# Kernel tuning notes

Measured on AMD Instinct MI355X. Metric: run time of the kernel, lower is better.

Reference implementation:

```python
import jax, jax.numpy as jnp
import numpy as np

B, S, D, N, H = 4, 1024, 768, 12, 64
IGNORE = -100000.0


def setup_inputs() -> dict:
    key = jax.random.key(0)
    ks = jax.random.split(key, 9)
    std = 0.02
    return {
        "normalized_resid_pre": jax.random.normal(ks[0], (B, S, D), dtype=jnp.float32),
        "W_Q": jax.random.normal(ks[1], (N, D, H), dtype=jnp.float32) * std,
        "W_K": jax.random.normal(ks[2], (N, D, H), dtype=jnp.float32) * std,
        "W_V": jax.random.normal(ks[3], (N, D, H), dtype=jnp.float32) * std,
        "W_O": jax.random.normal(ks[4], (N, H, D), dtype=jnp.float32) * std,
        "b_Q": jnp.zeros((N, H), dtype=jnp.float32),
        "b_K": jnp.zeros((N, H), dtype=jnp.float32),
        "b_V": jnp.zeros((N, H), dtype=jnp.float32),
        "b_O": jnp.zeros((D,), dtype=jnp.float32),
    }


def reference(normalized_resid_pre, W_Q, W_K, W_V, W_O, b_Q, b_K, b_V, b_O):
    x = normalized_resid_pre  # [b, s, d]
    d_head = W_Q.shape[-1]
    # per-head projections: [b, n, s, h]
    Q = jnp.einsum("bsd,ndh->bnsh", x, W_Q) + b_Q[None, :, None, :]
    K = jnp.einsum("bsd,ndh->bnsh", x, W_K) + b_K[None, :, None, :]
    V = jnp.einsum("bsd,ndh->bnsh", x, W_V) + b_V[None, :, None, :]
    # scores [b, n, s_q, s_k]
    scores = jnp.einsum("bnqh,bnkh->bnqk", Q, K) / jnp.sqrt(jnp.float32(d_head))
    s = scores.shape[-1]
    # original: tril(scores) + triu(IGNORE, k=1) == where(causal, scores, IGNORE)
    causal = jnp.tril(jnp.ones((s, s), dtype=bool))
    masked = jnp.where(causal[None, None], scores, jnp.float32(IGNORE))
    probs = jax.nn.softmax(masked, axis=-1)
    # z [b, s_q, n, h]
    z = jnp.einsum("bnqk,bnkh->bqnh", probs, V)
    out = jnp.einsum("bqnh,nhd->bqd", z, W_O) + b_O
    return out
```

## Files before the change

### kernel.cpp

```cpp
#include <hip/hip_runtime.h>

typedef __bf16 bf16x8 __attribute__((ext_vector_type(8)));
typedef __bf16 bf16x4 __attribute__((ext_vector_type(4)));
typedef float  f32x4  __attribute__((ext_vector_type(4)));

constexpr int B_ = 4, S_ = 1024, D_ = 768, N_ = 12, H_ = 64;
constexpr int BNSH = B_ * N_ * S_ * H_;
constexpr float SCALE2 = 0.18033688011f;

__device__ __forceinline__ f32x4 mfma16(bf16x8 a, bf16x8 b, f32x4 c) {
    return __builtin_amdgcn_mfma_f32_16x16x32_bf16(a, b, c, 0, 0, 0);
}

__device__ __forceinline__ void gload16(const __bf16* g, __bf16* l) {
    __builtin_amdgcn_global_load_lds(
        (const __attribute__((address_space(1))) unsigned int*)g,
        (__attribute__((address_space(3))) unsigned int*)l, 16, 0, 0);
}

__device__ __forceinline__ void stage128x64(const __bf16* g, int ld, __bf16* lds,
                                            int wid, int lane) {
    #pragma unroll
    for (int i = 0; i < 4; ++i) {
        int cb = (wid * 4 + i) * 64;
        int chunk = cb + lane;
        int r = chunk >> 3, p = chunk & 7;
        int q = p ^ (r & 7);
        gload16(g + (size_t)r * ld + q * 8, lds + cb * 8);
    }
}
__device__ __forceinline__ void stage64x64(const __bf16* g, int ld, __bf16* lds,
                                           int wid, int lane) {
    #pragma unroll
    for (int i = 0; i < 2; ++i) {
        int cb = (wid * 2 + i) * 64;
        int chunk = cb + lane;
        int r = chunk >> 3, p = chunk & 7;
        int q = p ^ (r & 7);
        gload16(g + (size_t)r * ld + q * 8, lds + cb * 8);
    }
}

__global__ __launch_bounds__(256) void prep_kernel(
    const float* __restrict__ x,
    const float* __restrict__ wq, const float* __restrict__ wk,
    const float* __restrict__ wv, const float* __restrict__ wo,
    __bf16* __restrict__ xb, __bf16* __restrict__ wt, __bf16* __restrict__ wot) {
    __shared__ __bf16 T[64][65];
    const int blk = blockIdx.x;
    const int tid = threadIdx.x;
    if (blk < 768) {
        int base = blk * 1024 + tid;
        #pragma unroll
        for (int i = 0; i < 4; ++i) {
            int idx = base + i * 256;
            float4 v = ((const float4*)x)[idx];
            bf16x4 o;
            o[0] = (__bf16)v.x; o[1] = (__bf16)v.y;
            o[2] = (__bf16)v.z; o[3] = (__bf16)v.w;
            ((bf16x4*)xb)[idx] = o;
        }
        return;
    }
    int rr = tid >> 4, c4 = (tid & 15) * 4;
    if (blk < 1200) {
        int t = blk - 768;
        int dt = t % 12, mh = t / 12;
        int mat = mh / 12, n = mh % 12;
        const float* in = (mat == 0 ? wq : mat == 1 ? wk : wv) + (size_t)n * 768 * 64;
        __bf16* outp = wt + (size_t)(mat * 768 + n * 64) * 768;
        int d0 = dt * 64;
        #pragma unroll
        for (int i = 0; i < 4; ++i) {
            int row = rr + 16 * i;
            float4 v = *(const float4*)&in[(size_t)(d0 + row) * 64 + c4];
            T[c4 + 0][row] = (__bf16)v.x;
            T[c4 + 1][row] = (__bf16)v.y;
            T[c4 + 2][row] = (__bf16)v.z;
            T[c4 + 3][row] = (__bf16)v.w;
        }
        __syncthreads();
        #pragma unroll
        for (int i = 0; i < 4; ++i) {
            int hrow = rr + 16 * i;
            bf16x4 o;
            o[0] = T[hrow][c4 + 0]; o[1] = T[hrow][c4 + 1];
            o[2] = T[hrow][c4 + 2]; o[3] = T[hrow][c4 + 3];
            *(bf16x4*)&outp[(size_t)hrow * 768 + d0 + c4] = o;
        }
    } else {
        int t = blk - 1200;
        int r0 = (t % 12) * 64, c0 = (t / 12) * 64;
        #pragma unroll
        for (int i = 0; i < 4; ++i) {
            int row = rr + 16 * i;
            float4 v = *(const float4*)&wo[(size_t)(r0 + row) * 768 + c0 + c4];
            T[c4 + 0][row] = (__bf16)v.x;
            T[c4 + 1][row] = (__bf16)v.y;
            T[c4 + 2][row] = (__bf16)v.z;
            T[c4 + 3][row] = (__bf16)v.w;
        }
        __syncthreads();
        #pragma unroll
        for (int i = 0; i < 4; ++i) {
            int crow = rr + 16 * i;
            bf16x4 o;
            o[0] = T[crow][c4 + 0]; o[1] = T[crow][c4 + 1];
            o[2] = T[crow][c4 + 2]; o[3] = T[crow][c4 + 3];
            *(bf16x4*)&wot[(size_t)(c0 + crow) * 768 + r0 + c4] = o;
        }
    }
}

__global__ __launch_bounds__(256) void qkv_gemm(
    const __bf16* __restrict__ xb, const __bf16* __restrict__ wtg,
    const float* __restrict__ bq, const float* __restrict__ bk,
    const float* __restrict__ bv,
    __bf16* __restrict__ Qb, __bf16* __restrict__ Kb, __bf16* __restrict__ Vtb) {
    __shared__ __bf16 As[2][128 * 64];
    __shared__ __bf16 Bs[2][64 * 64];
    const int m0 = blockIdx.x * 128;
    const int j0 = blockIdx.y * 64;
    const int tid = threadIdx.x, wid = tid >> 6, lane = tid & 63;
    const int quad = lane >> 4, lrow = lane & 15;
    const int l3 = lrow & 7;
    int koff[2];
    #pragma unroll
    for (int ks = 0; ks < 2; ++ks)
        koff[ks] = lrow * 64 + ((ks * 4 + quad) ^ l3) * 8;

    f32x4 zf = {0.f, 0.f, 0.f, 0.f};
    f32x4 acc[2][4];
    #pragma unroll
    for (int i = 0; i < 2; ++i)
        #pragma unroll
        for (int j = 0; j < 4; ++j) acc[i][j] = zf;

    stage128x64(xb + (size_t)m0 * 768, 768, As[0], wid, lane);
    stage64x64(wtg + (size_t)j0 * 768, 768, Bs[0], wid, lane);

    for (int kt = 0; kt < 12; ++kt) {
        const int buf = kt & 1;
        __syncthreads();
        if (kt < 11) {
            stage128x64(xb + (size_t)m0 * 768 + (kt + 1) * 64, 768, As[buf ^ 1], wid, lane);
            stage64x64(wtg + (size_t)j0 * 768 + (kt + 1) * 64, 768, Bs[buf ^ 1], wid, lane);
        }
        #pragma unroll
        for (int ks = 0; ks < 2; ++ks) {
            bf16x8 af[2], bfr[4];
            #pragma unroll
            for (int mi = 0; mi < 2; ++mi)
                af[mi] = *(const bf16x8*)(As[buf] + (wid * 32 + mi * 16) * 64 + koff[ks]);
            #pragma unroll
            for (int ni = 0; ni < 4; ++ni)
                bfr[ni] = *(const bf16x8*)(Bs[buf] + ni * 1024 + koff[ks]);
            #pragma unroll
            for (int mi = 0; mi < 2; ++mi)
                #pragma unroll
                for (int ni = 0; ni < 4; ++ni)
                    acc[mi][ni] = mfma16(af[mi], bfr[ni], acc[mi][ni]);
        }
    }

    const int mat = j0 / 768;
    const int n = (j0 % 768) >> 6;
    const int b = m0 >> 10;
    const int s_base = (m0 & 1023) + wid * 32;
    const float* bias = (mat == 0 ? bq : mat == 1 ? bk : bv) + n * 64;
    const float osc = (mat == 0) ? SCALE2 : 1.0f;
    float bias_v[4];
    #pragma unroll
    for (int ni = 0; ni < 4; ++ni) bias_v[ni] = bias[ni * 16 + lrow];

    if (mat == 2) {
        __bf16* vout = Vtb + (size_t)(b * N_ + n) * 64 * 1024;
        #pragma unroll
        for (int mi = 0; mi < 2; ++mi)
            #pragma unroll
            for (int ni = 0; ni < 4; ++ni) {
                int h = ni * 16 + lrow;
                int s0 = s_base + mi * 16 + quad * 4;
                bf16x4 pv;
                #pragma unroll
                for (int r = 0; r < 4; ++r)
                    pv[r] = (__bf16)(acc[mi][ni][r] + bias_v[ni]);
                *(bf16x4*)(vout + (size_t)h * 1024 + s0) = pv;
            }
    } else {
        __bf16* qk = (mat == 0 ? Qb : Kb) + (size_t)(b * N_ + n) * 1024 * 64;
        #pragma unroll
        for (int mi = 0; mi < 2; ++mi)
            #pragma unroll
            for (int r = 0; r < 4; ++r) {
                int s = s_base + mi * 16 + quad * 4 + r;
                #pragma unroll
                for (int ni = 0; ni < 4; ++ni)
                    qk[(size_t)s * 64 + ni * 16 + lrow] =
                        (__bf16)((acc[mi][ni][r] + bias_v[ni]) * osc);
            }
    }
}

__global__ __launch_bounds__(256) void attn_mfma(
    const __bf16* __restrict__ Qb, const __bf16* __restrict__ Kb,
    const __bf16* __restrict__ Vtb, __bf16* __restrict__ zb) {
    __shared__ __bf16 Ks[2][64 * 64], Vs[2][64 * 64];
    __shared__ __bf16 Pt[4][16 * 64];
    const int bid = blockIdx.x;
    const int qt = 15 - bid / 48;
    const int bn = bid % 48;
    const int b = bn / N_, n = bn % N_;
    const int tid = threadIdx.x, wid = tid >> 6, lane = tid & 63;
    const int quad = lane >> 4, lrow = lane & 15;
    const int l3 = lrow & 7;
    const __bf16* Qg = Qb + (size_t)(b * N_ + n) * S_ * H_;
    const __bf16* Kg = Kb + (size_t)(b * N_ + n) * S_ * H_;
    const __bf16* Vg = Vtb + (size_t)(b * N_ + n) * H_ * S_;
    const int q0 = qt * 64;

    int koff[2];
    #pragma unroll
    for (int ks = 0; ks < 2; ++ks)
        koff[ks] = lrow * 64 + ((ks * 4 + quad) ^ l3) * 8;
    int ptw[4], ptr_[2];
    #pragma unroll
    for (int nt = 0; nt < 4; ++nt) {
        int c16 = nt * 2 + (quad >> 1);
        ptw[nt] = lrow * 64 + (c16 ^ l3) * 8 + (quad & 1) * 4;
    }
    #pragma unroll
    for (int ks = 0; ks < 2; ++ks)
        ptr_[ks] = lrow * 64 + ((ks * 4 + quad) ^ l3) * 8;

    bf16x8 qf[2];
    #pragma unroll
    for (int ks = 0; ks < 2; ++ks)
        qf[ks] = *(const bf16x8*)&Qg[(size_t)(q0 + wid * 16 + lrow) * 64
                                     + ks * 32 + quad * 8];

    stage64x64(Kg, 64, Ks[0], wid, lane);
    stage64x64(Vg, 1024, Vs[0], wid, lane);

    f32x4 zf = {0.f, 0.f, 0.f, 0.f};
    f32x4 o[4];
    #pragma unroll
    for (int i = 0; i < 4; ++i) o[i] = zf;
    float l_r = 0.f;
    __bf16* Pw = Pt[wid];
    const int myq = wid * 16 + lrow;

    auto do_tile = [&](int buf, bool diag) {
        f32x4 sc[4];
        #pragma unroll
        for (int nt = 0; nt < 4; ++nt) sc[nt] = zf;
        #pragma unroll
        for (int ks = 0; ks < 2; ++ks) {
            #pragma unroll
            for (int nt = 0; nt < 4; ++nt) {
                bf16x8 kfr = *(const bf16x8*)(Ks[buf] + nt * 1024 + koff[ks]);
                sc[nt] = mfma16(kfr, qf[ks], sc[nt]);
            }
        }
        if (diag) {
            #pragma unroll
            for (int nt = 0; nt < 4; ++nt)
                #pragma unroll
                for (int r = 0; r < 4; ++r)
                    if ((nt * 16 + quad * 4 + r) > myq) sc[nt][r] = -1e30f;
        }
        float rs = 0.f;
        #pragma unroll
        for (int nt = 0; nt < 4; ++nt)
            #pragma unroll
            for (int r = 0; r < 4; ++r) {
                float p = __builtin_amdgcn_exp2f(sc[nt][r]);
                sc[nt][r] = p;
                rs += p;
            }
        l_r += rs;
        #pragma unroll
        for (int nt = 0; nt < 4; ++nt) {
            bf16x4 pk;
            #pragma unroll
            for (int r = 0; r < 4; ++r) pk[r] = (__bf16)sc[nt][r];
            *(bf16x4*)(Pw + ptw[nt]) = pk;
        }
        #pragma unroll
        for (int ks = 0; ks < 2; ++ks) {
            bf16x8 pf = *(const bf16x8*)(Pw + ptr_[ks]);
            #pragma unroll
            for (int ht = 0; ht < 4; ++ht) {
                bf16x8 vfr = *(const bf16x8*)(Vs[buf] + ht * 1024 + koff[ks]);
                o[ht] = mfma16(vfr, pf, o[ht]);
            }
        }
    };

    for (int kt = 0; kt < qt; ++kt) {
        __syncthreads();
        stage64x64(Kg + (size_t)(kt + 1) * 64 * 64, 64, Ks[(kt + 1) & 1], wid, lane);
        stage64x64(Vg + (kt + 1) * 64, 1024, Vs[(kt + 1) & 1], wid, lane);
        do_tile(kt & 1, false);
    }
    __syncthreads();
    do_tile(qt & 1, true);

    l_r += __shfl_xor(l_r, 16);
    l_r += __shfl_xor(l_r, 32);
    const float linv = 1.0f / l_r;
    __bf16* zout = zb + (size_t)b * S_ * 768 + (size_t)(q0 + myq) * 768 + n * 64;
    #pragma unroll
    for (int ht = 0; ht < 4; ++ht) {
        bf16x4 zo;
        #pragma unroll
        for (int r = 0; r < 4; ++r) zo[r] = (__bf16)(o[ht][r] * linv);
        *(bf16x4*)&zout[ht * 16 + quad * 4] = zo;
    }
}

__global__ __launch_bounds__(256) void out_gemm(
    const __bf16* __restrict__ zb, const __bf16* __restrict__ wot,
    const float* __restrict__ bo, float* __restrict__ out) {
    __shared__ __bf16 As[2][64 * 64];
    __shared__ __bf16 Bs[2][64 * 64];
    const int m0 = blockIdx.x * 64;
    const int j0 = blockIdx.y * 64;
    const int tid = threadIdx.x, wid = tid >> 6, lane = tid & 63;
    const int quad = lane >> 4, lrow = lane & 15;
    const int l3 = lrow & 7;
    int koff[2];
    #pragma unroll
    for (int ks = 0; ks < 2; ++ks)
        koff[ks] = lrow * 64 + ((ks * 4 + quad) ^ l3) * 8;

    f32x4 zf = {0.f, 0.f, 0.f, 0.f};
    f32x4 acc[4];
    #pragma unroll
    for (int j = 0; j < 4; ++j) acc[j] = zf;

    stage64x64(zb + (size_t)m0 * 768, 768, As[0], wid, lane);
    stage64x64(wot + (size_t)j0 * 768, 768, Bs[0], wid, lane);

    for (int kt = 0; kt < 12; ++kt) {
        const int buf = kt & 1;
        __syncthreads();
        if (kt < 11) {
            stage64x64(zb + (size_t)m0 * 768 + (kt + 1) * 64, 768, As[buf ^ 1], wid, lane);
            stage64x64(wot + (size_t)j0 * 768 + (kt + 1) * 64, 768, Bs[buf ^ 1], wid, lane);
        }
        #pragma unroll
        for (int ks = 0; ks < 2; ++ks) {
            bf16x8 af = *(const bf16x8*)(As[buf] + wid * 1024 + koff[ks]);
            #pragma unroll
            for (int ni = 0; ni < 4; ++ni) {
                bf16x8 bfr = *(const bf16x8*)(Bs[buf] + ni * 1024 + koff[ks]);
                acc[ni] = mfma16(af, bfr, acc[ni]);
            }
        }
    }

    float bias_v[4];
    #pragma unroll
    for (int ni = 0; ni < 4; ++ni) bias_v[ni] = bo[j0 + ni * 16 + lrow];
    #pragma unroll
    for (int r = 0; r < 4; ++r) {
        int m = m0 + wid * 16 + quad * 4 + r;
        #pragma unroll
        for (int ni = 0; ni < 4; ++ni)
            out[(size_t)m * 768 + j0 + ni * 16 + lrow] = acc[ni][r] + bias_v[ni];
    }
}

extern "C" void kernel_launch(void* const* d_in, const int* in_sizes, int n_in,
                              void* d_out, int out_size, void* d_ws, size_t ws_size,
                              hipStream_t stream) {
    const float* x  = (const float*)d_in[0];
    const float* wq = (const float*)d_in[1];
    const float* wk = (const float*)d_in[2];
    const float* wv = (const float*)d_in[3];
    const float* wo = (const float*)d_in[4];
    const float* bq = (const float*)d_in[5];
    const float* bk = (const float*)d_in[6];
    const float* bv = (const float*)d_in[7];
    const float* bo = (const float*)d_in[8];
    float* out = (float*)d_out;

    __bf16* p   = (__bf16*)d_ws;
    __bf16* xb  = p;  p += (size_t)4096 * 768;
    __bf16* wt  = p;  p += (size_t)2304 * 768;
    __bf16* wot = p;  p += (size_t)768 * 768;
    __bf16* Qb  = p;  p += (size_t)BNSH;
    __bf16* Kb  = p;  p += (size_t)BNSH;
    __bf16* Vtb = p;  p += (size_t)BNSH;
    __bf16* zb  = p;  p += (size_t)4096 * 768;

    prep_kernel<<<1344, 256, 0, stream>>>(x, wq, wk, wv, wo, xb, wt, wot);
    qkv_gemm<<<dim3(32, 36), 256, 0, stream>>>(xb, wt, bq, bk, bv, Qb, Kb, Vtb);
    attn_mfma<<<768, 256, 0, stream>>>(Qb, Kb, Vtb, zb);
    out_gemm<<<dim3(64, 12), 256, 0, stream>>>(zb, wot, bo, out);
}
```

Baseline: 140.1 us.

## Enlarge QKV GEMM tile to 128x128 with 2x2 warp grid and vectorized Q/K stores

The QKV projection GEMM moves from 128x64 tiles to 128x128 tiles. Each of the four waves now computes a 64x64 subtile in a 2x2 arrangement, which raises register reuse and halves the grid. Double-buffered LDS staging is dropped in favour of a single buffer with two barriers per k-step. For Q/K the MFMA operands are swapped so each lane holds contiguous head elements, which allows bf16x4 vector stores instead of scalar stores. The risks are lost load/compute overlap, fewer blocks (576) to fill the GPU, and higher register pressure.

```diff
diff --git a/kernel.cpp b/kernel.cpp
--- a/kernel.cpp
+++ b/kernel.cpp
@@ -117,66 +117,58 @@
     const float* __restrict__ bq, const float* __restrict__ bk,
     const float* __restrict__ bv,
     __bf16* __restrict__ Qb, __bf16* __restrict__ Kb, __bf16* __restrict__ Vtb) {
-    __shared__ __bf16 As[2][128 * 64];
-    __shared__ __bf16 Bs[2][64 * 64];
+    __shared__ __bf16 As[128 * 64];
+    __shared__ __bf16 Bs[128 * 64];
     const int m0 = blockIdx.x * 128;
-    const int j0 = blockIdx.y * 64;
+    const int j0 = blockIdx.y * 128;
     const int tid = threadIdx.x, wid = tid >> 6, lane = tid & 63;
     const int quad = lane >> 4, lrow = lane & 15;
     const int l3 = lrow & 7;
+    const int wr = wid & 1, wc = wid >> 1;
     int koff[2];
     #pragma unroll
     for (int ks = 0; ks < 2; ++ks)
         koff[ks] = lrow * 64 + ((ks * 4 + quad) ^ l3) * 8;
 
+    const int mat = j0 / 768;
+    const int n_w = ((j0 + wc * 64) % 768) >> 6;
+    const int b = m0 >> 10;
+    const int s_base = (m0 & 1023) + wr * 64;
+    const float* bias = (mat == 0 ? bq : mat == 1 ? bk : bv) + n_w * 64;
+
     f32x4 zf = {0.f, 0.f, 0.f, 0.f};
-    f32x4 acc[2][4];
-    #pragma unroll
-    for (int i = 0; i < 2; ++i)
-        #pragma unroll
-        for (int j = 0; j < 4; ++j) acc[i][j] = zf;
-
-    stage128x64(xb + (size_t)m0 * 768, 768, As[0], wid, lane);
-    stage64x64(wtg + (size_t)j0 * 768, 768, Bs[0], wid, lane);
-
-    for (int kt = 0; kt < 12; ++kt) {
-        const int buf = kt & 1;
-        __syncthreads();
-        if (kt < 11) {
-            stage128x64(xb + (size_t)m0 * 768 + (kt + 1) * 64, 768, As[buf ^ 1], wid, lane);
-            stage64x64(wtg + (size_t)j0 * 768 + (kt + 1) * 64, 768, Bs[buf ^ 1], wid, lane);
-        }
-        #pragma unroll
-        for (int ks = 0; ks < 2; ++ks) {
-            bf16x8 af[2], bfr[4];
-            #pragma unroll
-            for (int mi = 0; mi < 2; ++mi)
-                af[mi] = *(const bf16x8*)(As[buf] + (wid * 32 + mi * 16) * 64 + koff[ks]);
-            #pragma unroll
-            for (int ni = 0; ni < 4; ++ni)
-                bfr[ni] = *(const bf16x8*)(Bs[buf] + ni * 1024 + koff[ks]);
-            #pragma unroll
-            for (int mi = 0; mi < 2; ++mi)
+    f32x4 acc[16];
+    #pragma unroll
+    for (int i = 0; i < 16; ++i) acc[i] = zf;
+
+    if (mat == 2) {
+        for (int kt = 0; kt < 12; ++kt) {
+            __syncthreads();
+            stage128x64(xb + (size_t)m0 * 768 + kt * 64, 768, As, wid, lane);
+            stage128x64(wtg + (size_t)j0 * 768 + kt * 64, 768, Bs, wid, lane);
+            __syncthreads();
+            #pragma unroll
+            for (int ks = 0; ks < 2; ++ks) {
+                bf16x8 af[4], bfr[4];
+                #pragma unroll
+                for (int mi = 0; mi < 4; ++mi)
+                    af[mi] = *(const bf16x8*)(As + (wr * 64 + mi * 16) * 64 + koff[ks]);
                 #pragma unroll
                 for (int ni = 0; ni < 4; ++ni)
-                    acc[mi][ni] = mfma16(af[mi], bfr[ni], acc[mi][ni]);
-        }
-    }
-
-    const int mat = j0 / 768;
-    const int n = (j0 % 768) >> 6;
-    const int b = m0 >> 10;
-    const int s_base = (m0 & 1023) + wid * 32;
-    const float* bias = (mat == 0 ? bq : mat == 1 ? bk : bv) + n * 64;
-    const float osc = (mat == 0) ? SCALE2 : 1.0f;
-    float bias_v[4];
-    #pragma unroll
-    for (int ni = 0; ni < 4; ++ni) bias_v[ni] = bias[ni * 16 + lrow];
-
-    if (mat == 2) {
-        __bf16* vout = Vtb + (size_t)(b * N_ + n) * 64 * 1024;
-        #pragma unroll
-        for (int mi = 0; mi < 2; ++mi)
+                    bfr[ni] = *(const bf16x8*)(Bs + (wc * 64 + ni * 16) * 64 + koff[ks]);
+                #pragma unroll
+                for (int mi = 0; mi < 4; ++mi)
+                    #pragma unroll
+                    for (int ni = 0; ni < 4; ++ni)
+                        acc[mi * 4 + ni] = mfma16(af[mi], bfr[ni], acc[mi * 4 + ni]);
+            }
+        }
+        float bias_v[4];
+        #pragma unroll
+        for (int ni = 0; ni < 4; ++ni) bias_v[ni] = bias[ni * 16 + lrow];
+        __bf16* vout = Vtb + (size_t)(b * N_ + n_w) * 64 * 1024;
+        #pragma unroll
+        for (int mi = 0; mi < 4; ++mi)
             #pragma unroll
             for (int ni = 0; ni < 4; ++ni) {
                 int h = ni * 16 + lrow;
@@ -184,21 +176,51 @@
                 bf16x4 pv;
                 #pragma unroll
                 for (int r = 0; r < 4; ++r)
-                    pv[r] = (__bf16)(acc[mi][ni][r] + bias_v[ni]);
+                    pv[r] = (__bf16)(acc[mi * 4 + ni][r] + bias_v[ni]);
                 *(bf16x4*)(vout + (size_t)h * 1024 + s0) = pv;
             }
     } else {
-        __bf16* qk = (mat == 0 ? Qb : Kb) + (size_t)(b * N_ + n) * 1024 * 64;
-        #pragma unroll
-        for (int mi = 0; mi < 2; ++mi)
-            #pragma unroll
-            for (int r = 0; r < 4; ++r) {
-                int s = s_base + mi * 16 + quad * 4 + r;
+        for (int kt = 0; kt < 12; ++kt) {
+            __syncthreads();
+            stage128x64(xb + (size_t)m0 * 768 + kt * 64, 768, As, wid, lane);
+            stage128x64(wtg + (size_t)j0 * 768 + kt * 64, 768, Bs, wid, lane);
+            __syncthreads();
+            #pragma unroll
+            for (int ks = 0; ks < 2; ++ks) {
+                bf16x8 af[4], bfr[4];
+                #pragma unroll
+                for (int mi = 0; mi < 4; ++mi)
+                    af[mi] = *(const bf16x8*)(As + (wr * 64 + mi * 16) * 64 + koff[ks]);
                 #pragma unroll
                 for (int ni = 0; ni < 4; ++ni)
-                    qk[(size_t)s * 64 + ni * 16 + lrow] =
-                        (__bf16)((acc[mi][ni][r] + bias_v[ni]) * osc);
-            }
+                    bfr[ni] = *(const bf16x8*)(Bs + (wc * 64 + ni * 16) * 64 + koff[ks]);
+                #pragma unroll
+                for (int ni = 0; ni < 4; ++ni)
+                    #pragma unroll
+                    for (int mi = 0; mi < 4; ++mi)
+                        acc[ni * 4 + mi] = mfma16(bfr[ni], af[mi], acc[ni * 4 + mi]);
+            }
+        }
+        const float osc = (mat == 0) ? SCALE2 : 1.0f;
+        float4 b4[4];
+        #pragma unroll
+        for (int ni = 0; ni < 4; ++ni)
+            b4[ni] = *(const float4*)&bias[ni * 16 + quad * 4];
+        __bf16* qk = (mat == 0 ? Qb : Kb) + (size_t)(b * N_ + n_w) * 1024 * 64;
+        #pragma unroll
+        for (int mi = 0; mi < 4; ++mi) {
+            int s = s_base + mi * 16 + lrow;
+            #pragma unroll
+            for (int ni = 0; ni < 4; ++ni) {
+                bf16x4 pk;
+                #pragma unroll
+                for (int r = 0; r < 4; ++r) {
+                    float bv_ = (&b4[ni].x)[r];
+                    pk[r] = (__bf16)((acc[ni * 4 + mi][r] + bv_) * osc);
+                }
+                *(bf16x4*)&qk[(size_t)s * 64 + ni * 16 + quad * 4] = pk;
+            }
+        }
     }
 }
 
@@ -396,7 +418,7 @@
     __bf16* zb  = p;  p += (size_t)4096 * 768;
 
     prep_kernel<<<1344, 256, 0, stream>>>(x, wq, wk, wv, wo, xb, wt, wot);
-    qkv_gemm<<<dim3(32, 36), 256, 0, stream>>>(xb, wt, bq, bk, bv, Qb, Kb, Vtb);
+    qkv_gemm<<<dim3(32, 18), 256, 0, stream>>>(xb, wt, bq, bk, bv, Qb, Kb, Vtb);
     attn_mfma<<<768, 256, 0, stream>>>(Qb, Kb, Vtb, zb);
     out_gemm<<<dim3(64, 12), 256, 0, stream>>>(zb, wot, bo, out);
 }
```

Measured after the change: 151.8 us. 8.3% more time.
